# Kernel optimization log

Hardware: AMD Instinct MI355X
Metric: run time of the kernel (lower is better)

Reference implementation:

```python
import jax, jax.numpy as jnp
import numpy as np

D_Z = 1024
D_MODEL = 4096
EPS = 1e-5  # torch LayerNorm default
CLAMP = 3.0


def setup_inputs() -> dict:
    key = jax.random.key(0)
    k_z, k_w, k_b = jax.random.split(key, 3)
    z = jax.random.normal(k_z, (8, 2048, D_Z), dtype=jnp.float32)
    # LayerNorm params (gamma=1, beta=0 init in torch; keep learnable form)
    ln_gamma = jnp.ones((D_Z,), dtype=jnp.float32)
    ln_beta = jnp.zeros((D_Z,), dtype=jnp.float32)
    # Linear: torch default init U(-1/sqrt(d_z), 1/sqrt(d_z))
    bound = 1.0 / np.sqrt(D_Z)
    W = jax.random.uniform(k_w, (D_Z, D_MODEL), minval=-bound, maxval=bound, dtype=jnp.float32)
    b = jax.random.uniform(k_b, (D_MODEL,), minval=-bound, maxval=bound, dtype=jnp.float32)
    scale = jnp.ones((1,), dtype=jnp.float32)
    return {"z": z, "ln_gamma": ln_gamma, "ln_beta": ln_beta, "W": W, "b": b, "scale": scale}


def reference(z, ln_gamma, ln_beta, W, b, scale):
    # LayerNorm over last dim
    mu = jnp.mean(z, axis=-1, keepdims=True)
    var = jnp.mean(jnp.square(z - mu), axis=-1, keepdims=True)
    zn = (z - mu) * jax.lax.rsqrt(var + EPS) * ln_gamma + ln_beta
    # Linear -> scalar scale -> tanh clamp
    x = (jnp.einsum('bsd,dm->bsm', zn, W) + b) * scale
    return jnp.tanh(x / CLAMP) * CLAMP
```

## Files before the change

kernel.cpp:

```cpp
#include <hip/hip_runtime.h>

#define M_DIM 16384
#define K_DIM 1024
#define N_DIM 4096
#define T_TILES (K_DIM / 64)

typedef __bf16 bf16x8 __attribute__((ext_vector_type(8)));
typedef float f32x16 __attribute__((ext_vector_type(16)));

__device__ __forceinline__ unsigned short f2bf(float f) {
    union { float f; unsigned int i; } v; v.f = f;
    unsigned int r = v.i + 0x7fffu + ((v.i >> 16) & 1u);
    return (unsigned short)(r >> 16);
}
__device__ __forceinline__ unsigned int pack2(float lo, float hi) {
    return ((unsigned int)f2bf(lo)) | (((unsigned int)f2bf(hi)) << 16);
}

__global__ __launch_bounds__(256) void prep_kernel(
        const float* __restrict__ z,
        const float* __restrict__ gamma,
        const float* __restrict__ beta,
        unsigned short* __restrict__ zn,
        const float* __restrict__ W,
        unsigned short* __restrict__ Wt) {
    __shared__ float t[32][33];
    const int tid = threadIdx.x;
    if (blockIdx.x < M_DIM / 4) {
        const int wave = tid >> 6;
        const int lane = tid & 63;
        const size_t row = (size_t)blockIdx.x * 4 + wave;
        const float* zr = z + row * K_DIM;

        float4 x[4];
#pragma unroll
        for (int v = 0; v < 4; v++) x[v] = *(const float4*)(zr + v * 256 + lane * 4);

        float s = 0.f, ss = 0.f;
#pragma unroll
        for (int v = 0; v < 4; v++) {
            s  += x[v].x + x[v].y + x[v].z + x[v].w;
            ss += x[v].x * x[v].x + x[v].y * x[v].y + x[v].z * x[v].z + x[v].w * x[v].w;
        }
#pragma unroll
        for (int o = 32; o; o >>= 1) { s += __shfl_xor(s, o, 64); ss += __shfl_xor(ss, o, 64); }
        const float mean = s * (1.f / K_DIM);
        const float var = ss * (1.f / K_DIM) - mean * mean;
        const float rstd = rsqrtf(var + 1e-5f);

#pragma unroll
        for (int v = 0; v < 4; v++) {
            float4 g = *(const float4*)(gamma + v * 256 + lane * 4);
            float4 b = *(const float4*)(beta + v * 256 + lane * 4);
            float o0 = (x[v].x - mean) * rstd * g.x + b.x;
            float o1 = (x[v].y - mean) * rstd * g.y + b.y;
            float o2 = (x[v].z - mean) * rstd * g.z + b.z;
            float o3 = (x[v].w - mean) * rstd * g.w + b.w;
            uint2 q; q.x = pack2(o0, o1); q.y = pack2(o2, o3);
            *(uint2*)(zn + row * K_DIM + v * 256 + lane * 4) = q;
        }
    } else {
        const int bid = blockIdx.x - M_DIM / 4;
        const int tx = tid & 31, ty = tid >> 5;
        const int n0 = (bid & (N_DIM / 32 - 1)) * 32, k0 = (bid / (N_DIM / 32)) * 32;
#pragma unroll
        for (int j = 0; j < 32; j += 8)
            t[ty + j][tx] = W[(size_t)(k0 + ty + j) * N_DIM + n0 + tx];
        __syncthreads();
#pragma unroll
        for (int j = 0; j < 32; j += 8)
            Wt[(size_t)(n0 + ty + j) * K_DIM + k0 + tx] = f2bf(t[tx][ty + j]);
    }
}

__device__ __forceinline__ void async_copy16(const unsigned short* g, unsigned short* l) {
    __builtin_amdgcn_global_load_lds(
        (const __attribute__((address_space(1))) unsigned int*)g,
        (__attribute__((address_space(3))) unsigned int*)l,
        16, 0, 0);
}

__global__ __launch_bounds__(512, 2) void gemm_kernel(
        const unsigned short* __restrict__ A,
        const unsigned short* __restrict__ B,
        const float* __restrict__ bias,
        const float* __restrict__ scale,
        float* __restrict__ out) {
    __shared__ __align__(16) unsigned short As[2][256 * 64];
    __shared__ __align__(16) unsigned short Bs[2][256 * 64];

    const int tid = threadIdx.x;
    const int wave = tid >> 6, lane = tid & 63;
    const int wm = wave >> 2, wn = wave & 3;
    const int l31 = lane & 31, lhi = lane >> 5;

    const int bid = blockIdx.y * gridDim.x + blockIdx.x;
    const int id2 = (bid & 7) * 128 + (bid >> 3);
    const int bm = id2 >> 4, bn = id2 & 15;

    const int r0 = tid >> 3;
    const int c0 = ((tid & 7) ^ ((tid >> 3) & 7)) << 3;
    const unsigned short* agA = A + (size_t)(bm * 256 + r0) * K_DIM + c0;
    const unsigned short* agB = B + (size_t)(bn * 256 + r0) * K_DIM + c0;
    const int ldsu = wave * 512;

#define STAGE(t_, s_) do { \
        const unsigned short* gA_ = agA + (t_) * 64; \
        const unsigned short* gB_ = agB + (t_) * 64; \
        async_copy16(gA_,                 &As[s_][ldsu]); \
        async_copy16(gA_ +  64 * K_DIM,   &As[s_][ldsu + 4096]); \
        async_copy16(gA_ + 128 * K_DIM,   &As[s_][ldsu + 8192]); \
        async_copy16(gA_ + 192 * K_DIM,   &As[s_][ldsu + 12288]); \
        async_copy16(gB_,                 &Bs[s_][ldsu]); \
        async_copy16(gB_ +  64 * K_DIM,   &Bs[s_][ldsu + 4096]); \
        async_copy16(gB_ + 128 * K_DIM,   &Bs[s_][ldsu + 8192]); \
        async_copy16(gB_ + 192 * K_DIM,   &Bs[s_][ldsu + 12288]); } while (0)

    f32x16 acc[4][2] = {};
    bf16x8 a[2][4], b[2][4];
    const int rsw = l31 & 7;

#define READ_A(s_, h_) do { \
        const unsigned short* as_ = As[s_]; \
        _Pragma("unroll") \
        for (int i_ = 0; i_ < 2; ++i_) \
        _Pragma("unroll") \
        for (int ks_ = 0; ks_ < 4; ++ks_) \
            a[i_][ks_] = *(const bf16x8*)&as_[(wm * 128 + (h_) * 64 + i_ * 32 + l31) * 64 + (((2 * ks_ + lhi) ^ rsw) << 3)]; } while (0)
#define READ_B(s_) do { \
        const unsigned short* bs_ = Bs[s_]; \
        _Pragma("unroll") \
        for (int j_ = 0; j_ < 2; ++j_) \
        _Pragma("unroll") \
        for (int ks_ = 0; ks_ < 4; ++ks_) \
            b[j_][ks_] = *(const bf16x8*)&bs_[(wn * 64 + j_ * 32 + l31) * 64 + (((2 * ks_ + lhi) ^ rsw) << 3)]; } while (0)

    STAGE(0, 0);
    STAGE(1, 1);
    asm volatile("s_waitcnt vmcnt(8)" ::: "memory");
    __builtin_amdgcn_s_barrier();
    asm volatile("" ::: "memory");

#pragma unroll 2
    for (int t = 0; t < T_TILES; ++t) {
        const int s = t & 1;

        READ_B(s);
        READ_A(s, 0);
        asm volatile("s_waitcnt lgkmcnt(0)" ::: "memory");
        __builtin_amdgcn_sched_barrier(0);
        __builtin_amdgcn_s_setprio(1);
#pragma unroll
        for (int ks = 0; ks < 4; ++ks)
#pragma unroll
            for (int i = 0; i < 2; ++i)
#pragma unroll
                for (int j = 0; j < 2; ++j)
                    acc[i][j] = __builtin_amdgcn_mfma_f32_32x32x16_bf16(a[i][ks], b[j][ks], acc[i][j], 0, 0, 0);
        __builtin_amdgcn_s_setprio(0);

        READ_A(s, 1);
        asm volatile("s_waitcnt lgkmcnt(0)" ::: "memory");
        __builtin_amdgcn_sched_barrier(0);
        __builtin_amdgcn_s_setprio(1);
#pragma unroll
        for (int ks = 0; ks < 4; ++ks)
#pragma unroll
            for (int i = 0; i < 2; ++i)
#pragma unroll
                for (int j = 0; j < 2; ++j)
                    acc[2 + i][j] = __builtin_amdgcn_mfma_f32_32x32x16_bf16(a[i][ks], b[j][ks], acc[2 + i][j], 0, 0, 0);
        __builtin_amdgcn_s_setprio(0);

        if (t < T_TILES - 1) {
            __builtin_amdgcn_s_barrier();
            asm volatile("" ::: "memory");
            if (t + 2 < T_TILES) {
                STAGE(t + 2, s);
                asm volatile("s_waitcnt vmcnt(8)" ::: "memory");
            } else {
                asm volatile("s_waitcnt vmcnt(0)" ::: "memory");
            }
            __builtin_amdgcn_s_barrier();
            asm volatile("" ::: "memory");
        }
    }
#undef STAGE
#undef READ_A
#undef READ_B

    const float mfac = scale[0] * 0.96179669392236f;
#pragma unroll
    for (int j = 0; j < 2; ++j) {
        const int gcol = bn * 256 + wn * 64 + j * 32 + l31;
        const float bv = bias[gcol];
#pragma unroll
        for (int i = 0; i < 4; ++i) {
            const int rbase = bm * 256 + wm * 128 + i * 32 + 4 * lhi;
#pragma unroll
            for (int r = 0; r < 16; ++r) {
                const int grow = rbase + (r & 3) + 8 * (r >> 2);
                float tv = (acc[i][j][r] + bv) * mfac;
                float e = __builtin_amdgcn_exp2f(tv);
                out[(size_t)grow * N_DIM + gcol] = 3.f - 6.f * __builtin_amdgcn_rcpf(e + 1.f);
            }
        }
    }
}

extern "C" void kernel_launch(void* const* d_in, const int* in_sizes, int n_in,
                              void* d_out, int out_size, void* d_ws, size_t ws_size,
                              hipStream_t stream) {
    const float* z     = (const float*)d_in[0];
    const float* gamma = (const float*)d_in[1];
    const float* beta  = (const float*)d_in[2];
    const float* W     = (const float*)d_in[3];
    const float* b     = (const float*)d_in[4];
    const float* scale = (const float*)d_in[5];
    float* out = (float*)d_out;

    unsigned short* zn = (unsigned short*)d_ws;
    unsigned short* Wt = zn + (size_t)M_DIM * K_DIM;

    prep_kernel<<<M_DIM / 4 + (N_DIM / 32) * (K_DIM / 32), 256, 0, stream>>>(z, gamma, beta, zn, W, Wt);
    gemm_kernel<<<dim3(N_DIM / 256, M_DIM / 256), 512, 0, stream>>>(zn, Wt, b, scale, out);
}
```

Before: 463.2 us.

## Software-pipeline LDS fragment reads with MFMA groups using partial lgkmcnt waits

Splits each K tile into two K-halves and four MFMA groups with separate register fragments. LDS reads for the next group, and the first fragments of the next tile, are issued before the current MFMA group runs. Partial lgkmcnt waits replace the full drains, and the global stage of tile t+2 is issued after the fragment reads of the current buffer complete. This is meant to hide LDS latency behind MFMA work, at the cost of more registers and a vmcnt(0) wait every iteration that may expose global load latency.

Measured after the change: 489.2 us. 5.6% more time.

```diff
diff --git a/kernel.cpp b/kernel.cpp
--- a/kernel.cpp
+++ b/kernel.cpp
@@ -117,77 +117,92 @@
         async_copy16(gB_ + 192 * K_DIM,   &Bs[s_][ldsu + 12288]); } while (0)
 
     f32x16 acc[4][2] = {};
-    bf16x8 a[2][4], b[2][4];
+    bf16x8 a0[2][2], a1[2][2], a2[2][2], a3[2][2], b0[2][2], b1[2][2];
     const int rsw = l31 & 7;
 
-#define READ_A(s_, h_) do { \
+#define RA(dst_, s_, h_, kp_) do { \
         const unsigned short* as_ = As[s_]; \
         _Pragma("unroll") \
         for (int i_ = 0; i_ < 2; ++i_) \
         _Pragma("unroll") \
-        for (int ks_ = 0; ks_ < 4; ++ks_) \
-            a[i_][ks_] = *(const bf16x8*)&as_[(wm * 128 + (h_) * 64 + i_ * 32 + l31) * 64 + (((2 * ks_ + lhi) ^ rsw) << 3)]; } while (0)
-#define READ_B(s_) do { \
+        for (int q_ = 0; q_ < 2; ++q_) \
+            dst_[i_][q_] = *(const bf16x8*)&as_[(wm * 128 + (h_) * 64 + i_ * 32 + l31) * 64 + ((((kp_) * 4 + q_ * 2 + lhi) ^ rsw) << 3)]; } while (0)
+#define RB(dst_, s_, kp_) do { \
         const unsigned short* bs_ = Bs[s_]; \
         _Pragma("unroll") \
         for (int j_ = 0; j_ < 2; ++j_) \
         _Pragma("unroll") \
-        for (int ks_ = 0; ks_ < 4; ++ks_) \
-            b[j_][ks_] = *(const bf16x8*)&bs_[(wn * 64 + j_ * 32 + l31) * 64 + (((2 * ks_ + lhi) ^ rsw) << 3)]; } while (0)
+        for (int q_ = 0; q_ < 2; ++q_) \
+            dst_[j_][q_] = *(const bf16x8*)&bs_[(wn * 64 + j_ * 32 + l31) * 64 + ((((kp_) * 4 + q_ * 2 + lhi) ^ rsw) << 3)]; } while (0)
+#define MFG(r_, aa_, bb_) do { \
+        _Pragma("unroll") \
+        for (int q_ = 0; q_ < 2; ++q_) \
+        _Pragma("unroll") \
+        for (int i_ = 0; i_ < 2; ++i_) \
+        _Pragma("unroll") \
+        for (int j_ = 0; j_ < 2; ++j_) \
+            acc[(r_) + i_][j_] = __builtin_amdgcn_mfma_f32_32x32x16_bf16(aa_[i_][q_], bb_[j_][q_], acc[(r_) + i_][j_], 0, 0, 0); } while (0)
 
     STAGE(0, 0);
     STAGE(1, 1);
     asm volatile("s_waitcnt vmcnt(8)" ::: "memory");
     __builtin_amdgcn_s_barrier();
     asm volatile("" ::: "memory");
+    RA(a0, 0, 0, 0); RB(b0, 0, 0);
 
 #pragma unroll 2
     for (int t = 0; t < T_TILES; ++t) {
         const int s = t & 1;
 
-        READ_B(s);
-        READ_A(s, 0);
-        asm volatile("s_waitcnt lgkmcnt(0)" ::: "memory");
-        __builtin_amdgcn_sched_barrier(0);
-        __builtin_amdgcn_s_setprio(1);
-#pragma unroll
-        for (int ks = 0; ks < 4; ++ks)
-#pragma unroll
-            for (int i = 0; i < 2; ++i)
-#pragma unroll
-                for (int j = 0; j < 2; ++j)
-                    acc[i][j] = __builtin_amdgcn_mfma_f32_32x32x16_bf16(a[i][ks], b[j][ks], acc[i][j], 0, 0, 0);
-        __builtin_amdgcn_s_setprio(0);
-
-        READ_A(s, 1);
-        asm volatile("s_waitcnt lgkmcnt(0)" ::: "memory");
-        __builtin_amdgcn_sched_barrier(0);
-        __builtin_amdgcn_s_setprio(1);
-#pragma unroll
-        for (int ks = 0; ks < 4; ++ks)
-#pragma unroll
-            for (int i = 0; i < 2; ++i)
-#pragma unroll
-                for (int j = 0; j < 2; ++j)
-                    acc[2 + i][j] = __builtin_amdgcn_mfma_f32_32x32x16_bf16(a[i][ks], b[j][ks], acc[2 + i][j], 0, 0, 0);
-        __builtin_amdgcn_s_setprio(0);
-
-        if (t < T_TILES - 1) {
+        RA(a2, s, 1, 0);
+        RA(a1, s, 0, 1); RB(b1, s, 1);
+
+        asm volatile("s_waitcnt lgkmcnt(12)" ::: "memory");
+        __builtin_amdgcn_sched_barrier(0);
+        __builtin_amdgcn_s_setprio(1);
+        MFG(0, a0, b0);
+        __builtin_amdgcn_s_setprio(0);
+
+        asm volatile("s_waitcnt lgkmcnt(8)" ::: "memory");
+        __builtin_amdgcn_sched_barrier(0);
+        __builtin_amdgcn_s_setprio(1);
+        MFG(2, a2, b0);
+        __builtin_amdgcn_s_setprio(0);
+
+        RA(a3, s, 1, 1);
+        if (t + 1 < T_TILES) {
+            asm volatile("s_waitcnt vmcnt(0)" ::: "memory");
             __builtin_amdgcn_s_barrier();
             asm volatile("" ::: "memory");
-            if (t + 2 < T_TILES) {
-                STAGE(t + 2, s);
-                asm volatile("s_waitcnt vmcnt(8)" ::: "memory");
-            } else {
-                asm volatile("s_waitcnt vmcnt(0)" ::: "memory");
-            }
+            RA(a0, s ^ 1, 0, 0); RB(b0, s ^ 1, 0);
+            asm volatile("s_waitcnt lgkmcnt(12)" ::: "memory");
+        } else {
+            asm volatile("s_waitcnt lgkmcnt(4)" ::: "memory");
+        }
+        __builtin_amdgcn_sched_barrier(0);
+        __builtin_amdgcn_s_setprio(1);
+        MFG(0, a1, b1);
+        __builtin_amdgcn_s_setprio(0);
+
+        if (t + 1 < T_TILES) {
+            asm volatile("s_waitcnt lgkmcnt(8)" ::: "memory");
+        } else {
+            asm volatile("s_waitcnt lgkmcnt(0)" ::: "memory");
+        }
+        __builtin_amdgcn_sched_barrier(0);
+        if (t + 2 < T_TILES) {
             __builtin_amdgcn_s_barrier();
             asm volatile("" ::: "memory");
-        }
+            STAGE(t + 2, s);
+        }
+        __builtin_amdgcn_s_setprio(1);
+        MFG(2, a3, b1);
+        __builtin_amdgcn_s_setprio(0);
     }
 #undef STAGE
-#undef READ_A
-#undef READ_B
+#undef RA
+#undef RB
+#undef MFG
 
     const float mfac = scale[0] * 0.96179669392236f;
 #pragma unroll
```
